# Kernel tuning notes

Hardware: AMD Instinct MI355X
Metric: run time of the kernel (lower is better)

Reference implementation:

```python
import jax, jax.numpy as jnp
import numpy as np

B, N_IN, N_OUT = 4096, 2048, 2048


def setup_inputs() -> dict:
    key = jax.random.key(0)
    ks = jax.random.split(key, 11)
    s = 1.0 / np.sqrt(N_IN + N_OUT)  # torch Linear default-ish scale
    return {
        "c_old": jax.random.normal(ks[0], (B, N_OUT), jnp.float32),
        "h_old": jax.random.normal(ks[1], (B, N_OUT), jnp.float32),
        "x": jax.random.normal(ks[2], (B, N_IN), jnp.float32),
        "Wf": jax.random.normal(ks[3], (N_OUT, N_IN + N_OUT), jnp.float32) * s,
        "bf": jax.random.normal(ks[4], (N_OUT,), jnp.float32) * s,
        "Wi": jax.random.normal(ks[5], (N_OUT, N_IN + N_OUT), jnp.float32) * s,
        "bi": jax.random.normal(ks[6], (N_OUT,), jnp.float32) * s,
        "Wo": jax.random.normal(ks[7], (N_OUT, N_IN + N_OUT), jnp.float32) * s,
        "bo": jax.random.normal(ks[8], (N_OUT,), jnp.float32) * s,
        "Wg": jax.random.normal(ks[9], (N_OUT, N_IN + N_OUT), jnp.float32) * s,
        "bg": jax.random.normal(ks[10], (N_OUT,), jnp.float32) * s,
        "mode": 0,  # 0 = 'encode' (decode path is identical math with separate params)
    }


def reference(c_old, h_old, x, Wf, bf, Wi, bi, Wo, bo, Wg, bg, mode):
    # tensor = cat([x, h_old]) along the feature axis: [B, n_in + n_out]
    t = jnp.concatenate([x, h_old], axis=-1)
    # Fuse the 4 gate linears into one GEMM: [B, 4*n_out]
    W = jnp.concatenate([Wf, Wi, Wo, Wg], axis=0)
    b = jnp.concatenate([bf, bi, bo, bg], axis=0)
    gates = t @ W.T + b
    zf, zi, zo, zg = jnp.split(gates, 4, axis=-1)
    f = jax.nn.sigmoid(zf)
    i = jax.nn.sigmoid(zi)
    o = jax.nn.sigmoid(zo)
    g = jnp.tanh(zg)
    c = f * c_old + i * g
    h = o * jnp.tanh(c)
    return (c, h)
```

## Files before the change

kernel.cpp:

```cpp
#include <hip/hip_runtime.h>
#include <cstdint>


#define B_DIM 4096
#define NIN   2048
#define NOUT  2048
#define K_DIM 4096
#define NG    8192

#define BM 256
#define BN 256
#define BK 64
#define NT      (K_DIM / BK)
#define NSTREAM (NT * 4)

typedef __attribute__((ext_vector_type(8))) short bf16x8;
typedef __attribute__((ext_vector_type(4))) float f32x4;

__device__ inline unsigned short f2bf(float f) {
    uint32_t u = __float_as_uint(f);
    uint32_t r = (u + 0x7fffu + ((u >> 16) & 1u)) >> 16;
    return (unsigned short)r;
}

__device__ inline float sel4(float a, float b, float c, float d, int s) {
    float x = (s & 1) ? b : a;
    float y = (s & 1) ? d : c;
    return (s & 2) ? y : x;
}

#define TBLK ((B_DIM * K_DIM / 8) / 256)
#define WBLK ((NG * K_DIM / 8) / 256)
__global__ void pack_kernel(const float* __restrict__ x,
                            const float* __restrict__ h_old,
                            const float* __restrict__ Wf, const float* __restrict__ Wi,
                            const float* __restrict__ Wo, const float* __restrict__ Wg,
                            unsigned short* __restrict__ t,
                            unsigned short* __restrict__ Wp) {
    const float* src;
    unsigned short* dst;
    int idx;
    if (blockIdx.x < TBLK) {
        idx = blockIdx.x * 256 + threadIdx.x;
        int b = idx >> 9;
        int k = (idx & 511) << 3;
        src = (k < NIN) ? (x + (size_t)b * NIN + k)
                        : (h_old + (size_t)b * NOUT + (k - NIN));
        dst = t;
    } else {
        idx = (blockIdx.x - TBLK) * 256 + threadIdx.x;
        int row = idx >> 9;
        int k = (idx & 511) << 3;
        int jf = row >> 2, q = row & 3;
        src = ((q == 0) ? Wf : (q == 1) ? Wi : (q == 2) ? Wo : Wg)
              + (size_t)jf * K_DIM + k;
        dst = Wp;
    }
    float4 lo = ((const float4*)src)[0];
    float4 hi = ((const float4*)src)[1];
    uint4 o;
    o.x = f2bf(lo.x) | ((uint32_t)f2bf(lo.y) << 16);
    o.y = f2bf(lo.z) | ((uint32_t)f2bf(lo.w) << 16);
    o.z = f2bf(hi.x) | ((uint32_t)f2bf(hi.y) << 16);
    o.w = f2bf(hi.z) | ((uint32_t)f2bf(hi.w) << 16);
    ((uint4*)dst)[idx] = o;
}

#define GL2LDS(g, l) \
    __builtin_amdgcn_global_load_lds((const __attribute__((address_space(1))) void*)(g), \
                                     (__attribute__((address_space(3))) void*)(l), 16, 0, 0)

#define ASM_VMCNT4() asm volatile("s_waitcnt vmcnt(4)" ::: "memory")
#define ASM_VMCNT0() asm volatile("s_waitcnt vmcnt(0)" ::: "memory")
#define ASM_LGKM0()  asm volatile("s_waitcnt lgkmcnt(0)" ::: "memory")
#define BAR()        __builtin_amdgcn_s_barrier()

#define STAGE(idx_) do {                                                          \
    const int _i = (idx_);                                                        \
    if (_i < NSTREAM) {                                                           \
        const int _tile = _i >> 2;                                                \
        const int _h    = (_i >> 1) & 1;                                          \
        const int _buf  = _tile & 1;                                              \
        const unsigned short* _g = ((_i & 1) ? Wg : Tg)                           \
                                   + (size_t)(_h * 128) * K_DIM + _tile * BK;     \
        unsigned short* _l = ((_i & 1) ? Bs : As)                                 \
                             + _buf * (BM * BK) + _h * 8192 + ldst;               \
        GL2LDS(_g, _l);                                                           \
        GL2LDS(_g + (size_t)64 * K_DIM, _l + 4096);                               \
    }                                                                             \
} while (0)

__global__ __launch_bounds__(512, 1)
void lstm_gemm_kernel(const unsigned short* __restrict__ T,
                      const unsigned short* __restrict__ Wp,
                      const float* __restrict__ bf_, const float* __restrict__ bi_,
                      const float* __restrict__ bo_, const float* __restrict__ bg_,
                      const float* __restrict__ c_old,
                      float* __restrict__ c_out, float* __restrict__ h_out) {
    __shared__ __align__(16) unsigned short As[2 * BM * BK];
    __shared__ __align__(16) unsigned short Bs[2 * BN * BK];

    const int tid  = threadIdx.x;
    const int lane = tid & 63;
    const int w    = tid >> 6;
    const int wr   = w >> 2;
    const int wc   = w & 3;

    const int bid = blockIdx.x;
    const int swz = (bid & 7) * 64 + (bid >> 3);
    const int m0  = (swz >> 5) * BM;
    const int n0  = (swz & 31) * BN;

    const int rloc = tid >> 3;
    const int coff = ((tid & 7) ^ ((tid >> 3) & 7)) << 3;
    const unsigned short* Tg = T  + (size_t)(m0 + rloc) * K_DIM + coff;
    const unsigned short* Wg = Wp + (size_t)(n0 + rloc) * K_DIM + coff;
    const int ldst = tid * 8;

    const int rsel = lane & 15, ksel = lane >> 4;
    const int cs0 = (ksel)     ^ (lane & 7);
    const int cs1 = (4 + ksel) ^ (lane & 7);
    const int aidx = (wr * 128 + rsel) * 8;
    const int bidx = (wc * 64  + rsel) * 8;

    const bf16x8* Av = (const bf16x8*)As;
    const bf16x8* Bv = (const bf16x8*)Bs;

    f32x4 acc[8][4];
#pragma unroll
    for (int i = 0; i < 8; ++i)
#pragma unroll
        for (int j = 0; j < 4; ++j)
            acc[i][j] = (f32x4){0.f, 0.f, 0.f, 0.f};

    STAGE(0); STAGE(1); STAGE(2); STAGE(3); STAGE(4); STAGE(5);
    ASM_VMCNT4();
    BAR();

    bf16x8 a0[4][2], a1[4][2], bfr[2][2];

#pragma unroll 2
    for (int t = 0; t < NT; ++t) {
        const int bo = (t & 1) * 2048;

        STAGE(4 * t + 6);
#pragma unroll
        for (int i = 0; i < 4; ++i) {
            a0[i][0] = Av[bo + aidx + i * 128 + cs0];
            a0[i][1] = Av[bo + aidx + i * 128 + cs1];
        }
#pragma unroll
        for (int j = 0; j < 2; ++j) {
            bfr[j][0] = Bv[bo + bidx + j * 128 + cs0];
            bfr[j][1] = Bv[bo + bidx + j * 128 + cs1];
        }
        BAR();
        ASM_LGKM0();
        __builtin_amdgcn_s_setprio(1);
#pragma unroll
        for (int s = 0; s < 2; ++s)
#pragma unroll
            for (int i = 0; i < 4; ++i)
#pragma unroll
                for (int j = 0; j < 2; ++j)
                    acc[i][j] = __builtin_amdgcn_mfma_f32_16x16x32_bf16(
                        a0[i][s], bfr[j][s], acc[i][j], 0, 0, 0);
        __builtin_amdgcn_s_setprio(0);
        BAR();

        STAGE(4 * t + 7);
#pragma unroll
        for (int i = 0; i < 4; ++i) {
            a1[i][0] = Av[bo + aidx + 512 + i * 128 + cs0];
            a1[i][1] = Av[bo + aidx + 512 + i * 128 + cs1];
        }
        BAR();
        ASM_LGKM0();
        __builtin_amdgcn_s_setprio(1);
#pragma unroll
        for (int s = 0; s < 2; ++s)
#pragma unroll
            for (int i = 0; i < 4; ++i)
#pragma unroll
                for (int j = 0; j < 2; ++j)
                    acc[4 + i][j] = __builtin_amdgcn_mfma_f32_16x16x32_bf16(
                        a1[i][s], bfr[j][s], acc[4 + i][j], 0, 0, 0);
        __builtin_amdgcn_s_setprio(0);
        BAR();

        STAGE(4 * t + 8);
#pragma unroll
        for (int j = 0; j < 2; ++j) {
            bfr[j][0] = Bv[bo + bidx + 256 + j * 128 + cs0];
            bfr[j][1] = Bv[bo + bidx + 256 + j * 128 + cs1];
        }
        BAR();
        ASM_LGKM0();
        __builtin_amdgcn_s_setprio(1);
#pragma unroll
        for (int s = 0; s < 2; ++s)
#pragma unroll
            for (int i = 0; i < 4; ++i)
#pragma unroll
                for (int j = 0; j < 2; ++j)
                    acc[4 + i][2 + j] = __builtin_amdgcn_mfma_f32_16x16x32_bf16(
                        a1[i][s], bfr[j][s], acc[4 + i][2 + j], 0, 0, 0);
        __builtin_amdgcn_s_setprio(0);
        BAR();

        STAGE(4 * t + 9);
        BAR();
        __builtin_amdgcn_s_setprio(1);
#pragma unroll
        for (int s = 0; s < 2; ++s)
#pragma unroll
            for (int i = 0; i < 4; ++i)
#pragma unroll
                for (int j = 0; j < 2; ++j)
                    acc[i][2 + j] = __builtin_amdgcn_mfma_f32_16x16x32_bf16(
                        a0[i][s], bfr[j][s], acc[i][2 + j], 0, 0, 0);
        __builtin_amdgcn_s_setprio(0);
        if (t < NT - 2) { ASM_VMCNT4(); } else { ASM_VMCNT0(); }
        BAR();
    }

    const int q = lane & 3;
    const float* bsrc = (q == 0) ? bf_ : (q == 1) ? bi_ : (q == 2) ? bo_ : bg_;
    const int colbase = n0 + wc * 64 + (lane & 15);
    float bias[4];
#pragma unroll
    for (int j = 0; j < 4; ++j)
        bias[j] = bsrc[(colbase + 16 * j) >> 2];

    const int rowbase = m0 + wr * 128 + 4 * (lane >> 4);
#pragma unroll
    for (int i = 0; i < 8; ++i) {
#pragma unroll
        for (int j = 0; j < 4; ++j) {
            const int featbase = (n0 + wc * 64 + 16 * j) >> 2;
#pragma unroll
            for (int r = 0; r < 4; ++r) {
                float z = acc[i][j][r] + bias[j];
                float v;
                if (q == 3) {
                    v = 1.f - 2.f / (__expf(2.f * z) + 1.f);
                } else {
                    v = 1.f / (1.f + __expf(-z));
                }
                float v1 = __shfl_xor(v, 1);
                float v2 = __shfl_xor(v, 2);
                float v3 = __shfl_xor(v, 3);
                float fg = sel4(v, v1, v2, v3, q);
                float ig = sel4(v, v1, v2, v3, q ^ 1);
                float og = sel4(v, v1, v2, v3, q ^ 2);
                float gg = sel4(v, v1, v2, v3, q ^ 3);
                if ((lane & 3) == r) {
                    const int row  = rowbase + 16 * i + r;
                    const int feat = featbase + ((lane & 15) >> 2);
                    const size_t off = (size_t)row * NOUT + feat;
                    float co = c_old[off];
                    float c  = fg * co + ig * gg;
                    float h  = og * (1.f - 2.f / (__expf(2.f * c) + 1.f));
                    c_out[off] = c;
                    h_out[off] = h;
                }
            }
        }
    }
}

extern "C" void kernel_launch(void* const* d_in, const int* in_sizes, int n_in,
                              void* d_out, int out_size, void* d_ws, size_t ws_size,
                              hipStream_t stream) {
    const float* c_old = (const float*)d_in[0];
    const float* h_old = (const float*)d_in[1];
    const float* x     = (const float*)d_in[2];
    const float* Wf    = (const float*)d_in[3];
    const float* bf_   = (const float*)d_in[4];
    const float* Wi    = (const float*)d_in[5];
    const float* bi_   = (const float*)d_in[6];
    const float* Wo    = (const float*)d_in[7];
    const float* bo_   = (const float*)d_in[8];
    const float* Wg    = (const float*)d_in[9];
    const float* bg_   = (const float*)d_in[10];

    unsigned short* t  = (unsigned short*)d_ws;
    unsigned short* Wp = (unsigned short*)d_ws + (size_t)B_DIM * K_DIM;

    float* c_out = (float*)d_out;
    float* h_out = (float*)d_out + (size_t)B_DIM * NOUT;

    pack_kernel<<<TBLK + WBLK, 256, 0, stream>>>(x, h_old, Wf, Wi, Wo, Wg, t, Wp);

    lstm_gemm_kernel<<<dim3((B_DIM / BM) * (NG / BN)), dim3(512), 0, stream>>>(
        t, Wp, bf_, bi_, bo_, bg_, c_old, c_out, h_out);
}
```

Measured before the change: 630.0 us.

## Use hardware bf16 pack, nontemporal IO, new XCD tile map, reorder staging and MFMA

Several independent tweaks. The pack kernel now converts with v_cvt_pk_bf16_f32 and reads through nontemporal loads, and the epilogue reads c_old and writes c and h nontemporally. The block-to-tile mapping groups each XCD's blocks into an 8x8 patch of the output so tiles on one XCD share more of A and B in L2. In the main loop, global-to-LDS staging is issued after the LDS fragment reads, and the MFMA loop order now runs the two K halves back to back per accumulator. These can help cache reuse and issue overlap, but the MFMA reorder creates dependent back-to-back MFMAs on the same accumulator, which may stall.

```diff
diff --git a/kernel.cpp b/kernel.cpp
--- a/kernel.cpp
+++ b/kernel.cpp
@@ -16,11 +16,12 @@
 
 typedef __attribute__((ext_vector_type(8))) short bf16x8;
 typedef __attribute__((ext_vector_type(4))) float f32x4;
-
-__device__ inline unsigned short f2bf(float f) {
-    uint32_t u = __float_as_uint(f);
-    uint32_t r = (u + 0x7fffu + ((u >> 16) & 1u)) >> 16;
-    return (unsigned short)r;
+typedef __attribute__((ext_vector_type(4))) float fx4;
+
+__device__ inline uint32_t cvtpk(float a, float b) {
+    uint32_t r;
+    asm("v_cvt_pk_bf16_f32 %0, %1, %2" : "=v"(r) : "v"(a), "v"(b));
+    return r;
 }
 
 __device__ inline float sel4(float a, float b, float c, float d, int s) {
@@ -56,13 +57,13 @@
               + (size_t)jf * K_DIM + k;
         dst = Wp;
     }
-    float4 lo = ((const float4*)src)[0];
-    float4 hi = ((const float4*)src)[1];
+    fx4 lo = __builtin_nontemporal_load((const fx4*)src);
+    fx4 hi = __builtin_nontemporal_load(((const fx4*)src) + 1);
     uint4 o;
-    o.x = f2bf(lo.x) | ((uint32_t)f2bf(lo.y) << 16);
-    o.y = f2bf(lo.z) | ((uint32_t)f2bf(lo.w) << 16);
-    o.z = f2bf(hi.x) | ((uint32_t)f2bf(hi.y) << 16);
-    o.w = f2bf(hi.z) | ((uint32_t)f2bf(hi.w) << 16);
+    o.x = cvtpk(lo.x, lo.y);
+    o.y = cvtpk(lo.z, lo.w);
+    o.z = cvtpk(hi.x, hi.y);
+    o.w = cvtpk(hi.z, hi.w);
     ((uint4*)dst)[idx] = o;
 }
 
@@ -106,10 +107,13 @@
     const int wr   = w >> 2;
     const int wc   = w & 3;
 
-    const int bid = blockIdx.x;
-    const int swz = (bid & 7) * 64 + (bid >> 3);
-    const int m0  = (swz >> 5) * BM;
-    const int n0  = (swz & 31) * BN;
+    const int bid   = blockIdx.x;
+    const int xcd   = bid & 7;
+    const int intra = bid >> 3;
+    const int mi    = (xcd >> 2) * 8 + (intra & 7);
+    const int ni    = (xcd & 3) * 8 + (intra >> 3);
+    const int m0    = mi * BM;
+    const int n0    = ni * BN;
 
     const int rloc = tid >> 3;
     const int coff = ((tid & 7) ^ ((tid >> 3) & 7)) << 3;
@@ -143,7 +147,6 @@
     for (int t = 0; t < NT; ++t) {
         const int bo = (t & 1) * 2048;
 
-        STAGE(4 * t + 6);
 #pragma unroll
         for (int i = 0; i < 4; ++i) {
             a0[i][0] = Av[bo + aidx + i * 128 + cs0];
@@ -154,55 +157,56 @@
             bfr[j][0] = Bv[bo + bidx + j * 128 + cs0];
             bfr[j][1] = Bv[bo + bidx + j * 128 + cs1];
         }
+        STAGE(4 * t + 6);
         BAR();
         ASM_LGKM0();
         __builtin_amdgcn_s_setprio(1);
 #pragma unroll
-        for (int s = 0; s < 2; ++s)
-#pragma unroll
-            for (int i = 0; i < 4; ++i)
-#pragma unroll
-                for (int j = 0; j < 2; ++j)
+        for (int i = 0; i < 4; ++i)
+#pragma unroll
+            for (int j = 0; j < 2; ++j)
+#pragma unroll
+                for (int s = 0; s < 2; ++s)
                     acc[i][j] = __builtin_amdgcn_mfma_f32_16x16x32_bf16(
                         a0[i][s], bfr[j][s], acc[i][j], 0, 0, 0);
         __builtin_amdgcn_s_setprio(0);
         BAR();
 
-        STAGE(4 * t + 7);
 #pragma unroll
         for (int i = 0; i < 4; ++i) {
             a1[i][0] = Av[bo + aidx + 512 + i * 128 + cs0];
             a1[i][1] = Av[bo + aidx + 512 + i * 128 + cs1];
         }
+        STAGE(4 * t + 7);
         BAR();
         ASM_LGKM0();
         __builtin_amdgcn_s_setprio(1);
 #pragma unroll
-        for (int s = 0; s < 2; ++s)
-#pragma unroll
-            for (int i = 0; i < 4; ++i)
-#pragma unroll
-                for (int j = 0; j < 2; ++j)
+        for (int i = 0; i < 4; ++i)
+#pragma unroll
+            for (int j = 0; j < 2; ++j)
+#pragma unroll
+                for (int s = 0; s < 2; ++s)
                     acc[4 + i][j] = __builtin_amdgcn_mfma_f32_16x16x32_bf16(
                         a1[i][s], bfr[j][s], acc[4 + i][j], 0, 0, 0);
         __builtin_amdgcn_s_setprio(0);
         BAR();
 
-        STAGE(4 * t + 8);
 #pragma unroll
         for (int j = 0; j < 2; ++j) {
             bfr[j][0] = Bv[bo + bidx + 256 + j * 128 + cs0];
             bfr[j][1] = Bv[bo + bidx + 256 + j * 128 + cs1];
         }
+        STAGE(4 * t + 8);
         BAR();
         ASM_LGKM0();
         __builtin_amdgcn_s_setprio(1);
 #pragma unroll
-        for (int s = 0; s < 2; ++s)
-#pragma unroll
-            for (int i = 0; i < 4; ++i)
-#pragma unroll
-                for (int j = 0; j < 2; ++j)
+        for (int i = 0; i < 4; ++i)
+#pragma unroll
+            for (int j = 0; j < 2; ++j)
+#pragma unroll
+                for (int s = 0; s < 2; ++s)
                     acc[4 + i][2 + j] = __builtin_amdgcn_mfma_f32_16x16x32_bf16(
                         a1[i][s], bfr[j][s], acc[4 + i][2 + j], 0, 0, 0);
         __builtin_amdgcn_s_setprio(0);
@@ -258,11 +262,11 @@
                     const int row  = rowbase + 16 * i + r;
                     const int feat = featbase + ((lane & 15) >> 2);
                     const size_t off = (size_t)row * NOUT + feat;
-                    float co = c_old[off];
+                    float co = __builtin_nontemporal_load(c_old + off);
                     float c  = fg * co + ig * gg;
                     float h  = og * (1.f - 2.f / (__expf(2.f * c) + 1.f));
-                    c_out[off] = c;
-                    h_out[off] = h;
+                    __builtin_nontemporal_store(c, c_out + off);
+                    __builtin_nontemporal_store(h, h_out + off);
                 }
             }
         }
```

Measured after the change: 638.4 us. No clear change (+1.3%).
